# Kernel optimization log

Measured on AMD Instinct MI355X. Metric: run time of the kernel, lower is better.

## Reference

```python
import jax, jax.numpy as jnp
import numpy as np

B, T = 128, 512
D_IN, D_OUT, H = 12, 320, 64


def _conv1d(x, w, b, dilation):
    # x: [B,C,T], w: [O,I,K]  (torch Conv1d layout), 'same' padding for odd receptive field
    k = w.shape[-1]
    pad = ((k - 1) * dilation + 1) // 2
    y = jax.lax.conv_general_dilated(x, w, (1,), [(pad, pad)], rhs_dilation=(dilation,),
                                     dimension_numbers=('NCH', 'OIH', 'NCH'))
    return y + b[None, :, None]


def _gelu(x):
    return jax.nn.gelu(x, approximate=False)  # torch F.gelu default (erf)


def _encoder(x, c0_1_w, c0_1_b, c0_2_w, c0_2_b, c1_p_w, c1_p_b, c1_1_w, c1_1_b, c1_2_w, c1_2_b):
    # TS2Vec DilatedConvEncoder, channels=[64, 320], kernel=3. x: [B,T,64] -> [B,T,320]
    h = x.transpose(0, 2, 1)  # [B,64,T]
    # block 0: 64->64, dilation 1, identity residual
    res = h
    t = _conv1d(_gelu(h), c0_1_w, c0_1_b, 1)
    t = _conv1d(_gelu(t), c0_2_w, c0_2_b, 1)
    h = t + res
    # block 1: 64->320, dilation 2, final -> 1x1 projector residual
    res = _conv1d(h, c1_p_w, c1_p_b, 1)
    t = _conv1d(_gelu(h), c1_1_w, c1_1_b, 2)
    t = _conv1d(_gelu(t), c1_2_w, c1_2_b, 2)
    h = t + res
    return h.transpose(0, 2, 1)  # [B,T,320]


def _gru_cell(x, h, wih, whh, bih, bhh):
    # torch.nn.GRUCell math
    gi = x @ wih.T + bih  # [B,3H]
    gh = h @ whh.T + bhh
    i_r, i_z, i_n = jnp.split(gi, 3, axis=-1)
    h_r, h_z, h_n = jnp.split(gh, 3, axis=-1)
    r = jax.nn.sigmoid(i_r + h_r)
    z = jax.nn.sigmoid(i_z + h_z)
    n = jnp.tanh(i_n + r * h_n)
    return (1.0 - z) * n + z * h


def setup_inputs() -> dict:
    key = jax.random.key(0)
    ks = iter(jax.random.split(key, 40))
    f = lambda shape, s=0.05: (jax.random.normal(next(ks), shape, dtype=jnp.float32) * s)
    inp = {
        'x1': jax.random.normal(next(ks), (B, T, D_IN), dtype=jnp.float32),
        'x2': jax.random.normal(next(ks), (B, T, D_IN), dtype=jnp.float32),
        'X1': jax.random.normal(next(ks), (B, T, D_IN), dtype=jnp.float32),
        'X2': jax.random.normal(next(ks), (B, T, D_IN), dtype=jnp.float32),
        'X': jax.random.normal(next(ks), (B, T, D_IN), dtype=jnp.float32),
        'w_in': f((D_IN, H)), 'b_in': f((H,)),
        'c0_1_w': f((H, H, 3)), 'c0_1_b': f((H,)),
        'c0_2_w': f((H, H, 3)), 'c0_2_b': f((H,)),
        'c1_p_w': f((D_OUT, H, 1)), 'c1_p_b': f((D_OUT,)),
        'c1_1_w': f((D_OUT, H, 3)), 'c1_1_b': f((D_OUT,)),
        'c1_2_w': f((D_OUT, D_OUT, 3)), 'c1_2_b': f((D_OUT,)),
        'ih_dense_w': f((D_OUT, 4 * D_OUT)), 'ih_dense_b': f((4 * D_OUT,)),
        'ih_proj_w': f((4 * D_OUT, D_IN)), 'ih_proj_b': f((D_IN,)),
        'fc_w': f((D_IN, D_OUT)), 'fc_b': f((D_OUT,)),
        'gru_wih': f((3 * H, D_OUT)), 'gru_whh': f((3 * H, H)),
        'gru_bih': f((3 * H,)), 'gru_bhh': f((3 * H,)),
        'out_w': f((H, D_OUT)), 'out_b': f((D_OUT,)),
        'fcr_w': f((D_OUT, D_IN)), 'fcr_b': f((D_IN,)),
    }
    return inp


def reference(x1, x2, X1, X2, X, w_in, b_in, c0_1_w, c0_1_b, c0_2_w, c0_2_b,
              c1_p_w, c1_p_b, c1_1_w, c1_1_b, c1_2_w, c1_2_b,
              ih_dense_w, ih_dense_b, ih_proj_w, ih_proj_b,
              fc_w, fc_b, gru_wih, gru_whh, gru_bih, gru_bhh,
              out_w, out_b, fcr_w, fcr_b):
    conv_p = (c0_1_w, c0_1_b, c0_2_w, c0_2_b, c1_p_w, c1_p_b, c1_1_w, c1_1_b, c1_2_w, c1_2_b)
    m1 = (x1 != 0).astype(jnp.int32)
    m2 = (x2 != 0).astype(jnp.int32)
    enc = lambda a: _encoder(a @ w_in + b_in, *conv_p)  # dropout = identity (deterministic ref)
    x_whole1 = enc(X1)
    x_whole2 = enc(X2)

    def interp(a):
        r = enc(a)
        h = jax.nn.relu(r @ ih_dense_w + ih_dense_b)
        return h @ ih_proj_w + ih_proj_b  # [B,T,D_IN]

    x_interp1 = interp(x1)
    x_interp2 = interp(x2)
    mask1 = (~jnp.isnan(x_interp1).any(-1)).astype(jnp.float32)  # [B,T]

    y1 = x_interp1 @ fc_w + fc_b  # [B,T,320] (self.fc applied to every step at once)
    y2 = x_interp2 @ fc_w + fc_b
    h0 = jnp.zeros((x1.shape[0], gru_whh.shape[1]), x1.dtype)

    def step(carry, xs):
        h1, h2 = carry
        yt1, yt2, mt = xs
        h1 = _gru_cell(yt1, h1, gru_wih, gru_whh, gru_bih, gru_bhh)
        h2 = _gru_cell(yt2, h2, gru_wih, gru_whh, gru_bih, gru_bhh)
        o1 = h1 @ out_w + out_b
        o2 = h2 @ out_w + out_b
        keep = (mt == 1.0)[:, None]
        o1 = jnp.where(keep, yt1, o1)
        o2 = jnp.where(keep, yt1, o2)  # faithful: source uses mask1 / y_t1 for both
        return (h1, h2), (o1, o2)

    _, (o1, o2) = jax.lax.scan(step, (h0, h0),
                               (y1.transpose(1, 0, 2), y2.transpose(1, 0, 2), mask1.T))
    outputs2 = jax.lax.stop_gradient(o2.transpose(1, 0, 2)) @ fcr_w + fcr_b
    outputs1 = jax.lax.stop_gradient(o1.transpose(1, 0, 2)) @ fcr_w + fcr_b
    return (x_whole1, x_whole2, outputs1, outputs2, m1, m2, x1, x2)
```

## Files before the change

### kernel.cpp

```cpp
#include <hip/hip_runtime.h>
#include <hip/hip_bf16.h>
#include <math.h>


#define BB    128
#define TSEQ  512
#define NTILE 8
#define DIN   12
#define C0    64
#define C1    320
#define TT    64
#define PP    76
#define HALO  6
#define R64P  72

#define S1 ((size_t)BB * TSEQ * C1)
#define S2 ((size_t)BB * TSEQ * DIN)

typedef __attribute__((ext_vector_type(8))) __bf16 bf16x8;
typedef __attribute__((ext_vector_type(4))) float f32x4;
#define MFMA16(a, b, c) __builtin_amdgcn_mfma_f32_16x16x32_bf16(a, b, c, 0, 0, 0)

#define O01 0
#define O02 12288
#define O11 24576
#define O12 86016
#define OD  413696
#define OP  823296
#define NWS 843776
#define OGM 843776
#define OF2 844064

#define LA  0
#define LB  10656
#define LC  10656
#define LSZ 54176
#define LRR 0
#define LZB 40960
#define LXI 50176
#define LGM 53248
#define LF2 53824

__device__ __forceinline__ float bf2f(const __hip_bfloat16 v) { return __bfloat162float(v); }
__device__ __forceinline__ __hip_bfloat16 f2bf(float f)       { return __float2bfloat16(f); }
__device__ __forceinline__ float geluf(float x) {
    return 0.5f * x * (1.0f + erff(x * 0.7071067811865475f));
}
__device__ __forceinline__ bf16x8 ldb8(const void* p) { return *(const bf16x8*)p; }
__device__ __forceinline__ void* swp(void* base, int row, int col) {
    return (void*)((unsigned char*)base + (((row * 640 + col * 2)) ^ ((row & 7) << 4)));
}

extern "C" __global__ void __launch_bounds__(256) prep_w(
    const float* __restrict__ c01w, const float* __restrict__ c02w,
    const float* __restrict__ c11w, const float* __restrict__ c12w,
    const float* __restrict__ c1pw, const float* __restrict__ dw,
    const float* __restrict__ pw,
    const float* __restrict__ fcw,  const float* __restrict__ fcb,
    const float* __restrict__ fcrw, const float* __restrict__ fcrb,
    __hip_bfloat16* __restrict__ ws)
{
    for (size_t i = (size_t)blockIdx.x * 256 + threadIdx.x; i < NWS;
         i += (size_t)gridDim.x * 256) {
        float v;
        if (i < O02)      { int q = (int)i;        int n = q / 192, r = q % 192;
                            v = c01w[(n * 64 + (r & 63)) * 3 + (r >> 6)]; }
        else if (i < O11) { int q = (int)(i - O02); int n = q / 192, r = q % 192;
                            v = c02w[(n * 64 + (r & 63)) * 3 + (r >> 6)]; }
        else if (i < O12) { int q = (int)(i - O11); int n = q / 192, r = q % 192;
                            v = c11w[(n * 64 + (r & 63)) * 3 + (r >> 6)]; }
        else if (i < OD)  { int q = (int)(i - O12); int n = q >> 10, k = q & 1023;
                            v = (k < 960) ? c12w[(n * 320 + (k % 320)) * 3 + (k / 320)]
                                          : c1pw[n * 64 + (k - 960)]; }
        else if (i < OP)  { int q = (int)(i - OD);  int h = q / 320, c = q % 320;
                            v = dw[c * 1280 + h]; }
        else              { int q = (int)(i - OP);  int j = q / 1280, h = q % 1280;
                            v = (j < 12) ? pw[h * 12 + j] : 0.f; }
        ws[i] = f2bf(v);
    }
    if (blockIdx.x == 0) {
        float* gm = (float*)(ws + OGM);
        float* f2 = (float*)(ws + OF2);
        for (int o = threadIdx.x; o < 144; o += 256) {
            int j = o / 12, j2 = o - j * 12;
            float s = 0.f;
            for (int c = 0; c < C1; c++) s += fcw[j * C1 + c] * fcrw[c * 12 + j2];
            gm[o] = s;
        }
        if (threadIdx.x < 12) {
            float s = fcrb[threadIdx.x];
            for (int c = 0; c < C1; c++) s += fcb[c] * fcrw[c * 12 + threadIdx.x];
            f2[threadIdx.x] = s;
        }
    }
}

extern "C" __global__ void __launch_bounds__(256, 3) fused_main(
    const float* __restrict__ x1,  const float* __restrict__ X1,
    const float* __restrict__ X2,
    const float* __restrict__ w_in, const float* __restrict__ b_in,
    const float* __restrict__ c01b, const float* __restrict__ c02b,
    const float* __restrict__ c1pb, const float* __restrict__ c11b,
    const float* __restrict__ c12b,
    const float* __restrict__ db,   const float* __restrict__ pb,
    const __hip_bfloat16* __restrict__ ws,
    float* __restrict__ out)
{
    __shared__ __align__(16) unsigned char smem[LSZ];
    __hip_bfloat16* A  = (__hip_bfloat16*)(smem + LA);
    __hip_bfloat16* Bf = (__hip_bfloat16*)(smem + LB);
    unsigned char*  Cb = smem + LC;
    unsigned char*  Rb = smem + LRR;
    float* XI = (float*)(smem + LXI);
    float* Gm = (float*)(smem + LGM);
    float* F2 = (float*)(smem + LF2);

    const int tid  = threadIdx.x;
    const int wv   = tid >> 6;
    const int lane = tid & 63;
    const int lm   = lane & 15;
    const int lq   = lane >> 4;
    const int bid  = blockIdx.x;
    const int pass = bid % 3;
    const int rem  = bid / 3;
    const int b    = rem >> 3;
    const int t0   = (rem & (NTILE - 1)) * TT;
    const float* xin = (pass == 0) ? X1 : (pass == 1) ? X2 : x1;

    const f32x4 Z4 = {0.f, 0.f, 0.f, 0.f};

    for (int o = tid; o < PP * C0; o += 256) {
        int p = o >> 6, c = o & 63;
        int t = t0 + p - HALO;
        float acc = 0.f;
        if (t >= 0 && t < TSEQ) {
            acc = b_in[c];
            const float4* xr4 = (const float4*)(xin + ((size_t)b * TSEQ + t) * DIN);
            float4 v0 = xr4[0], v1 = xr4[1], v2 = xr4[2];
            const float xv[12] = {v0.x, v0.y, v0.z, v0.w, v1.x, v1.y,
                                  v1.z, v1.w, v2.x, v2.y, v2.z, v2.w};
            #pragma unroll
            for (int i = 0; i < DIN; i++) acc += xv[i] * w_in[i * C0 + c];
        }
        if (p < 74) A[p * R64P + c] = f2bf(acc);
        Bf[p * R64P + c] = f2bf(geluf(acc));
    }
    __syncthreads();

    {
        const int oc = wv * 16 + lm;
        bf16x8 bw[6];
        #pragma unroll
        for (int ks = 0; ks < 6; ks++)
            bw[ks] = ldb8(ws + O01 + oc * 192 + ks * 32 + (lq << 3));
        f32x4 acc[5] = {Z4, Z4, Z4, Z4, Z4};
        #pragma unroll
        for (int ks = 0; ks < 6; ks++) {
            int tap = ks >> 1, ci = ((ks & 1) << 5) + (lq << 3);
            #pragma unroll
            for (int mt = 0; mt < 5; mt++) {
                int p = 1 + mt * 16 + lm + tap - 1; p = p > 75 ? 75 : p;
                acc[mt] = MFMA16(ldb8(Bf + p * R64P + ci), bw[ks], acc[mt]);
            }
        }
        __syncthreads();
        float bias = c01b[oc];
        #pragma unroll
        for (int mt = 0; mt < 5; mt++)
            #pragma unroll
            for (int r = 0; r < 4; r++) {
                int m = mt * 16 + lq * 4 + r;
                if (m < 74) {
                    int p = 1 + m, t = t0 + p - HALO;
                    Bf[p * R64P + oc] =
                        f2bf((t >= 0 && t < TSEQ) ? geluf(acc[mt][r] + bias) : 0.f);
                }
            }
    }
    __syncthreads();

    {
        const int oc = wv * 16 + lm;
        bf16x8 bw[6];
        #pragma unroll
        for (int ks = 0; ks < 6; ks++)
            bw[ks] = ldb8(ws + O02 + oc * 192 + ks * 32 + (lq << 3));
        f32x4 acc[5] = {Z4, Z4, Z4, Z4, Z4};
        #pragma unroll
        for (int ks = 0; ks < 6; ks++) {
            int tap = ks >> 1, ci = ((ks & 1) << 5) + (lq << 3);
            #pragma unroll
            for (int mt = 0; mt < 5; mt++) {
                int p = 2 + mt * 16 + lm + tap - 1; p = p > 75 ? 75 : p;
                acc[mt] = MFMA16(ldb8(Bf + p * R64P + ci), bw[ks], acc[mt]);
            }
        }
        float resv[5][4];
        #pragma unroll
        for (int mt = 0; mt < 5; mt++)
            #pragma unroll
            for (int r = 0; r < 4; r++) {
                int m = mt * 16 + lq * 4 + r;
                resv[mt][r] = (m < 72) ? bf2f(A[(2 + m) * R64P + oc]) : 0.f;
            }
        __syncthreads();
        float bias = c02b[oc];
        #pragma unroll
        for (int mt = 0; mt < 5; mt++)
            #pragma unroll
            for (int r = 0; r < 4; r++) {
                int m = mt * 16 + lq * 4 + r;
                if (m < 72) {
                    int p = 2 + m, t = t0 + p - HALO;
                    bool v = (t >= 0 && t < TSEQ);
                    float hb = acc[mt][r] + bias + resv[mt][r];
                    A [p * R64P + oc] = f2bf(v ? hb : 0.f);
                    Bf[p * R64P + oc] = f2bf(v ? geluf(hb) : 0.f);
                }
            }
    }
    __syncthreads();

    {
        f32x4 acc[5][5];
        #pragma unroll
        for (int mt = 0; mt < 5; mt++)
            #pragma unroll
            for (int nt = 0; nt < 5; nt++) acc[mt][nt] = Z4;
        #pragma unroll
        for (int ks = 0; ks < 6; ks++) {
            int tap = ks >> 1, ci = ((ks & 1) << 5) + (lq << 3);
            bf16x8 a[5];
            #pragma unroll
            for (int mt = 0; mt < 5; mt++) {
                int p = 4 + mt * 16 + lm + 2 * (tap - 1); p = p > 75 ? 75 : p;
                a[mt] = ldb8(Bf + p * R64P + ci);
            }
            #pragma unroll
            for (int nt = 0; nt < 5; nt++) {
                bf16x8 bw = ldb8(ws + O11 + (wv * 80 + nt * 16 + lm) * 192
                                 + ks * 32 + (lq << 3));
                #pragma unroll
                for (int mt = 0; mt < 5; mt++)
                    acc[mt][nt] = MFMA16(a[mt], bw, acc[mt][nt]);
            }
        }
        __syncthreads();
        #pragma unroll
        for (int nt = 0; nt < 5; nt++) {
            int oc = wv * 80 + nt * 16 + lm;
            float bias = c11b[oc];
            #pragma unroll
            for (int mt = 0; mt < 5; mt++)
                #pragma unroll
                for (int r = 0; r < 4; r++) {
                    int m = mt * 16 + lq * 4 + r;
                    if (m < 68) {
                        int t = t0 + 4 + m - HALO;
                        *(__hip_bfloat16*)swp(Cb, m, oc) =
                            f2bf((t >= 0 && t < TSEQ) ? geluf(acc[mt][nt][r] + bias) : 0.f);
                    }
                }
        }
    }
    __syncthreads();

    {
        f32x4 acc[4][5];
        #pragma unroll
        for (int kk = 0; kk < 4; kk++)
            #pragma unroll
            for (int nt = 0; nt < 5; nt++) acc[kk][nt] = Z4;
        bf16x8 ba[5], bb[5];
        #pragma unroll
        for (int nt = 0; nt < 5; nt++)
            ba[nt] = ldb8(ws + O12 + (wv * 80 + nt * 16 + lm) * 1024 + (lq << 3));
        for (int ks = 0; ks < 32; ks += 2) {
            #pragma unroll
            for (int nt = 0; nt < 5; nt++)
                bb[nt] = ldb8(ws + O12 + (wv * 80 + nt * 16 + lm) * 1024
                              + (ks + 1) * 32 + (lq << 3));
            {
                bf16x8 a[4];
                if (ks < 30) {
                    int tap = (ks >= 20) ? 2 : (ks >= 10 ? 1 : 0);
                    int ci = (ks - tap * 10) * 32 + (lq << 3);
                    #pragma unroll
                    for (int mt = 0; mt < 4; mt++)
                        a[mt] = ldb8(swp(Cb, 2 + mt * 16 + lm + 2 * (tap - 1), ci));
                } else {
                    int ci = ((ks - 30) << 5) + (lq << 3);
                    #pragma unroll
                    for (int mt = 0; mt < 4; mt++)
                        a[mt] = ldb8(A + (6 + mt * 16 + lm) * R64P + ci);
                }
                #pragma unroll
                for (int nt = 0; nt < 5; nt++)
                    #pragma unroll
                    for (int mt = 0; mt < 4; mt++)
                        acc[mt][nt] = MFMA16(a[mt], ba[nt], acc[mt][nt]);
            }
            if (ks + 2 < 32)
                #pragma unroll
                for (int nt = 0; nt < 5; nt++)
                    ba[nt] = ldb8(ws + O12 + (wv * 80 + nt * 16 + lm) * 1024
                                  + (ks + 2) * 32 + (lq << 3));
            {
                int k1 = ks + 1;
                bf16x8 a[4];
                if (k1 < 30) {
                    int tap = (k1 >= 20) ? 2 : (k1 >= 10 ? 1 : 0);
                    int ci = (k1 - tap * 10) * 32 + (lq << 3);
                    #pragma unroll
                    for (int mt = 0; mt < 4; mt++)
                        a[mt] = ldb8(swp(Cb, 2 + mt * 16 + lm + 2 * (tap - 1), ci));
                } else {
                    int ci = ((k1 - 30) << 5) + (lq << 3);
                    #pragma unroll
                    for (int mt = 0; mt < 4; mt++)
                        a[mt] = ldb8(A + (6 + mt * 16 + lm) * R64P + ci);
                }
                #pragma unroll
                for (int nt = 0; nt < 5; nt++)
                    #pragma unroll
                    for (int mt = 0; mt < 4; mt++)
                        acc[mt][nt] = MFMA16(a[mt], bb[nt], acc[mt][nt]);
            }
        }
        if (pass < 2) {
            #pragma unroll
            for (int nt = 0; nt < 5; nt++) {
                int oc = wv * 80 + nt * 16 + lm;
                float bias = c12b[oc] + c1pb[oc];
                const size_t obase = (pass == 1) ? S1 : (size_t)0;
                #pragma unroll
                for (int mt = 0; mt < 4; mt++)
                    #pragma unroll
                    for (int r = 0; r < 4; r++) {
                        int m = mt * 16 + lq * 4 + r;
                        out[obase + ((size_t)b * TSEQ + t0 + m) * C1 + oc] =
                            acc[mt][nt][r] + bias;
                    }
            }
        } else {
            __syncthreads();
            #pragma unroll
            for (int nt = 0; nt < 5; nt++) {
                int oc = wv * 80 + nt * 16 + lm;
                float bias = c12b[oc] + c1pb[oc];
                #pragma unroll
                for (int mt = 0; mt < 4; mt++)
                    #pragma unroll
                    for (int r = 0; r < 4; r++) {
                        int m = mt * 16 + lq * 4 + r;
                        *(__hip_bfloat16*)swp(Rb, m, oc) = f2bf(acc[mt][nt][r] + bias);
                    }
            }
            const float* gmw = (const float*)(ws + OGM);
            const float* f2w = (const float*)(ws + OF2);
            for (int o = tid; o < TT * 12; o += 256) XI[o] = pb[o % 12];
            for (int o = tid; o < 144; o += 256) Gm[o] = gmw[o];
            if (tid < 12) F2[tid] = f2w[tid];
            __syncthreads();
        }
    }

    if (pass == 2) {
        __hip_bfloat16* zb = (__hip_bfloat16*)(smem + LZB) + wv * (16 * R64P);
        f32x4 xacc[4] = {Z4, Z4, Z4, Z4};
        for (int cn = 0; cn < 5; cn++) {
            const int h0 = wv * 320 + cn * 64;
            f32x4 dacc[4][4];
            #pragma unroll
            for (int mt = 0; mt < 4; mt++)
                #pragma unroll
                for (int nt = 0; nt < 4; nt++) dacc[mt][nt] = Z4;
            bf16x8 ba[4], bb[4];
            #pragma unroll
            for (int nt = 0; nt < 4; nt++)
                ba[nt] = ldb8(ws + OD + (h0 + nt * 16 + lm) * 320 + (lq << 3));
            for (int ks = 0; ks < 10; ks += 2) {
                #pragma unroll
                for (int nt = 0; nt < 4; nt++)
                    bb[nt] = ldb8(ws + OD + (h0 + nt * 16 + lm) * 320
                                  + (ks + 1) * 32 + (lq << 3));
                {
                    bf16x8 a[4];
                    #pragma unroll
                    for (int mt = 0; mt < 4; mt++)
                        a[mt] = ldb8(swp(Rb, mt * 16 + lm, ks * 32 + (lq << 3)));
                    #pragma unroll
                    for (int nt = 0; nt < 4; nt++)
                        #pragma unroll
                        for (int mt = 0; mt < 4; mt++)
                            dacc[mt][nt] = MFMA16(a[mt], ba[nt], dacc[mt][nt]);
                }
                if (ks + 2 < 10)
                    #pragma unroll
                    for (int nt = 0; nt < 4; nt++)
                        ba[nt] = ldb8(ws + OD + (h0 + nt * 16 + lm) * 320
                                      + (ks + 2) * 32 + (lq << 3));
                {
                    bf16x8 a[4];
                    #pragma unroll
                    for (int mt = 0; mt < 4; mt++)
                        a[mt] = ldb8(swp(Rb, mt * 16 + lm, (ks + 1) * 32 + (lq << 3)));
                    #pragma unroll
                    for (int nt = 0; nt < 4; nt++)
                        #pragma unroll
                        for (int mt = 0; mt < 4; mt++)
                            dacc[mt][nt] = MFMA16(a[mt], bb[nt], dacc[mt][nt]);
                }
            }
            #pragma unroll
            for (int mt = 0; mt < 4; mt++) {
                #pragma unroll
                for (int nt = 0; nt < 4; nt++) {
                    int h = h0 + nt * 16 + lm;
                    float dbv = db[h];
                    #pragma unroll
                    for (int r = 0; r < 4; r++)
                        zb[(lq * 4 + r) * R64P + nt * 16 + lm] =
                            f2bf(fmaxf(dacc[mt][nt][r] + dbv, 0.f));
                }
                #pragma unroll
                for (int k2 = 0; k2 < 2; k2++) {
                    int hl = k2 * 32 + (lq << 3);
                    bf16x8 bf = ldb8(ws + OP + lm * 1280 + h0 + hl);
                    xacc[mt] = MFMA16(ldb8(zb + lm * R64P + hl), bf, xacc[mt]);
                }
            }
        }
        if (lm < 12) {
            #pragma unroll
            for (int mt = 0; mt < 4; mt++)
                #pragma unroll
                for (int r = 0; r < 4; r++)
                    atomicAdd(&XI[(mt * 16 + lq * 4 + r) * 12 + lm], xacc[mt][r]);
        }
        __syncthreads();
        for (int o = tid; o < TT * 12; o += 256) {
            int p = o / 12, j2 = o - p * 12;
            float val = F2[j2];
            #pragma unroll
            for (int j = 0; j < 12; j++) val += XI[p * 12 + j] * Gm[j * 12 + j2];
            size_t idx = ((size_t)b * TSEQ + t0 + p) * DIN + j2;
            out[2 * S1 + idx]      = val;
            out[2 * S1 + S2 + idx] = val;
        }
    }
}

extern "C" __global__ void __launch_bounds__(256) tail_kernel(
    const float* __restrict__ x1, const float* __restrict__ x2,
    float* __restrict__ out)
{
    size_t i = (size_t)blockIdx.x * 256 + threadIdx.x;
    if (i >= S2) return;
    float a = x1[i], c = x2[i];
    const size_t base = 2 * S1 + 2 * S2;
    out[base + i]          = (a != 0.f) ? 1.f : 0.f;
    out[base + S2 + i]     = (c != 0.f) ? 1.f : 0.f;
    out[base + 2 * S2 + i] = a;
    out[base + 3 * S2 + i] = c;
}

extern "C" void kernel_launch(void* const* d_in, const int* in_sizes, int n_in,
                              void* d_out, int out_size, void* d_ws, size_t ws_size,
                              hipStream_t stream)
{
    (void)in_sizes; (void)n_in; (void)ws_size; (void)out_size;
    const float* x1   = (const float*)d_in[0];
    const float* x2   = (const float*)d_in[1];
    const float* X1   = (const float*)d_in[2];
    const float* X2   = (const float*)d_in[3];
    const float* w_in = (const float*)d_in[5];
    const float* b_in = (const float*)d_in[6];
    const float* c01w = (const float*)d_in[7];
    const float* c01b = (const float*)d_in[8];
    const float* c02w = (const float*)d_in[9];
    const float* c02b = (const float*)d_in[10];
    const float* c1pw = (const float*)d_in[11];
    const float* c1pb = (const float*)d_in[12];
    const float* c11w = (const float*)d_in[13];
    const float* c11b = (const float*)d_in[14];
    const float* c12w = (const float*)d_in[15];
    const float* c12b = (const float*)d_in[16];
    const float* dwp  = (const float*)d_in[17];
    const float* dbp  = (const float*)d_in[18];
    const float* pwp  = (const float*)d_in[19];
    const float* pbp  = (const float*)d_in[20];
    const float* fcw  = (const float*)d_in[21];
    const float* fcb  = (const float*)d_in[22];
    const float* fcrw = (const float*)d_in[29];
    const float* fcrb = (const float*)d_in[30];
    float* out = (float*)d_out;
    __hip_bfloat16* ws = (__hip_bfloat16*)d_ws;

    prep_w<<<824, 256, 0, stream>>>(c01w, c02w, c11w, c12w, c1pw, dwp, pwp,
                                    fcw, fcb, fcrw, fcrb, ws);

    fused_main<<<3 * BB * NTILE, 256, 0, stream>>>(
        x1, X1, X2, w_in, b_in, c01b, c02b, c1pb, c11b, c12b,
        dbp, pbp, ws, out);

    tail_kernel<<<(int)((S2 + 255) / 256), 256, 0, stream>>>(x1, x2, out);
}
```

Baseline: 933.9 us.

## Prefetch conv weights with deeper register pipelining and relocate pass-2 LDS buffers

Moves the XI/Gm/F2 shared buffers to a region of their own past the existing LDS layout, so they can be filled at kernel start for pass 2 rather than after the last conv. The first dilated conv now prefetches the next k-step's weight fragments into registers. The second conv moves to a triple-buffered weight / double-buffered activation software pipeline, so global weight loads overlap the MFMAs. The extra registers and LDS make the launch bound drop from 3 to 2 blocks per SM, which may reduce occupancy.

```diff
diff --git a/kernel.cpp b/kernel.cpp
--- a/kernel.cpp
+++ b/kernel.cpp
@@ -34,12 +34,12 @@
 #define LA  0
 #define LB  10656
 #define LC  10656
-#define LSZ 54176
+#define LXI 54176
+#define LGM 57248
+#define LF2 57824
+#define LSZ 57872
 #define LRR 0
 #define LZB 40960
-#define LXI 50176
-#define LGM 53248
-#define LF2 53824
 
 __device__ __forceinline__ float bf2f(const __hip_bfloat16 v) { return __bfloat162float(v); }
 __device__ __forceinline__ __hip_bfloat16 f2bf(float f)       { return __float2bfloat16(f); }
@@ -48,7 +48,7 @@
 }
 __device__ __forceinline__ bf16x8 ldb8(const void* p) { return *(const bf16x8*)p; }
 __device__ __forceinline__ void* swp(void* base, int row, int col) {
-    return (void*)((unsigned char*)base + (((row * 640 + col * 2)) ^ ((row & 7) << 4)));
+    return (void*)((unsigned char*)base + ((row * 640 + col * 2) ^ ((row & 7) << 4)));
 }
 
 extern "C" __global__ void __launch_bounds__(256) prep_w(
@@ -95,7 +95,7 @@
     }
 }
 
-extern "C" __global__ void __launch_bounds__(256, 3) fused_main(
+extern "C" __global__ void __launch_bounds__(256, 2) fused_main(
     const float* __restrict__ x1,  const float* __restrict__ X1,
     const float* __restrict__ X2,
     const float* __restrict__ w_in, const float* __restrict__ b_in,
@@ -129,6 +129,14 @@
 
     const f32x4 Z4 = {0.f, 0.f, 0.f, 0.f};
 
+    if (pass == 2) {
+        const float* gmw = (const float*)(ws + OGM);
+        const float* f2w = (const float*)(ws + OF2);
+        for (int o = tid; o < 144; o += 256) Gm[o] = gmw[o];
+        if (tid < 12) F2[tid] = f2w[tid];
+        for (int o = tid; o < TT * 12; o += 256) XI[o] = pb[o % 12];
+    }
+
     for (int o = tid; o < PP * C0; o += 256) {
         int p = o >> 6, c = o & 63;
         int t = t0 + p - HALO;
@@ -227,8 +235,17 @@
         for (int mt = 0; mt < 5; mt++)
             #pragma unroll
             for (int nt = 0; nt < 5; nt++) acc[mt][nt] = Z4;
+        bf16x8 bcur[5], bnxt[5];
+        #pragma unroll
+        for (int nt = 0; nt < 5; nt++)
+            bcur[nt] = ldb8(ws + O11 + (wv * 80 + nt * 16 + lm) * 192 + (lq << 3));
         #pragma unroll
         for (int ks = 0; ks < 6; ks++) {
+            if (ks < 5)
+                #pragma unroll
+                for (int nt = 0; nt < 5; nt++)
+                    bnxt[nt] = ldb8(ws + O11 + (wv * 80 + nt * 16 + lm) * 192
+                                    + (ks + 1) * 32 + (lq << 3));
             int tap = ks >> 1, ci = ((ks & 1) << 5) + (lq << 3);
             bf16x8 a[5];
             #pragma unroll
@@ -237,13 +254,12 @@
                 a[mt] = ldb8(Bf + p * R64P + ci);
             }
             #pragma unroll
-            for (int nt = 0; nt < 5; nt++) {
-                bf16x8 bw = ldb8(ws + O11 + (wv * 80 + nt * 16 + lm) * 192
-                                 + ks * 32 + (lq << 3));
+            for (int nt = 0; nt < 5; nt++)
                 #pragma unroll
                 for (int mt = 0; mt < 5; mt++)
-                    acc[mt][nt] = MFMA16(a[mt], bw, acc[mt][nt]);
-            }
+                    acc[mt][nt] = MFMA16(a[mt], bcur[nt], acc[mt][nt]);
+            #pragma unroll
+            for (int nt = 0; nt < 5; nt++) bcur[nt] = bnxt[nt];
         }
         __syncthreads();
         #pragma unroll
@@ -268,65 +284,50 @@
     {
         f32x4 acc[4][5];
         #pragma unroll
-        for (int kk = 0; kk < 4; kk++)
-            #pragma unroll
-            for (int nt = 0; nt < 5; nt++) acc[kk][nt] = Z4;
-        bf16x8 ba[5], bb[5];
-        #pragma unroll
-        for (int nt = 0; nt < 5; nt++)
-            ba[nt] = ldb8(ws + O12 + (wv * 80 + nt * 16 + lm) * 1024 + (lq << 3));
-        for (int ks = 0; ks < 32; ks += 2) {
+        for (int mt = 0; mt < 4; mt++)
+            #pragma unroll
+            for (int nt = 0; nt < 5; nt++) acc[mt][nt] = Z4;
+        bf16x8 a0[4], a1[4], b0[5], b1[5], b2[5];
+        auto LDA = [&](int ks, bf16x8 (&a)[4]) {
+            if (ks < 30) {
+                int tap = (ks >= 20) ? 2 : (ks >= 10 ? 1 : 0);
+                int ci = (ks - tap * 10) * 32 + (lq << 3);
+                #pragma unroll
+                for (int mt = 0; mt < 4; mt++)
+                    a[mt] = ldb8(swp(Cb, 2 + mt * 16 + lm + 2 * (tap - 1), ci));
+            } else {
+                int ci = ((ks - 30) << 5) + (lq << 3);
+                #pragma unroll
+                for (int mt = 0; mt < 4; mt++)
+                    a[mt] = ldb8(A + (6 + mt * 16 + lm) * R64P + ci);
+            }
+        };
+        auto LDB = [&](int ks, bf16x8 (&bw)[5]) {
             #pragma unroll
             for (int nt = 0; nt < 5; nt++)
-                bb[nt] = ldb8(ws + O12 + (wv * 80 + nt * 16 + lm) * 1024
-                              + (ks + 1) * 32 + (lq << 3));
-            {
-                bf16x8 a[4];
-                if (ks < 30) {
-                    int tap = (ks >= 20) ? 2 : (ks >= 10 ? 1 : 0);
-                    int ci = (ks - tap * 10) * 32 + (lq << 3);
-                    #pragma unroll
-                    for (int mt = 0; mt < 4; mt++)
-                        a[mt] = ldb8(swp(Cb, 2 + mt * 16 + lm + 2 * (tap - 1), ci));
-                } else {
-                    int ci = ((ks - 30) << 5) + (lq << 3);
-                    #pragma unroll
-                    for (int mt = 0; mt < 4; mt++)
-                        a[mt] = ldb8(A + (6 + mt * 16 + lm) * R64P + ci);
-                }
-                #pragma unroll
-                for (int nt = 0; nt < 5; nt++)
-                    #pragma unroll
-                    for (int mt = 0; mt < 4; mt++)
-                        acc[mt][nt] = MFMA16(a[mt], ba[nt], acc[mt][nt]);
-            }
-            if (ks + 2 < 32)
-                #pragma unroll
-                for (int nt = 0; nt < 5; nt++)
-                    ba[nt] = ldb8(ws + O12 + (wv * 80 + nt * 16 + lm) * 1024
-                                  + (ks + 2) * 32 + (lq << 3));
-            {
-                int k1 = ks + 1;
-                bf16x8 a[4];
-                if (k1 < 30) {
-                    int tap = (k1 >= 20) ? 2 : (k1 >= 10 ? 1 : 0);
-                    int ci = (k1 - tap * 10) * 32 + (lq << 3);
-                    #pragma unroll
-                    for (int mt = 0; mt < 4; mt++)
-                        a[mt] = ldb8(swp(Cb, 2 + mt * 16 + lm + 2 * (tap - 1), ci));
-                } else {
-                    int ci = ((k1 - 30) << 5) + (lq << 3);
-                    #pragma unroll
-                    for (int mt = 0; mt < 4; mt++)
-                        a[mt] = ldb8(A + (6 + mt * 16 + lm) * R64P + ci);
-                }
-                #pragma unroll
-                for (int nt = 0; nt < 5; nt++)
-                    #pragma unroll
-                    for (int mt = 0; mt < 4; mt++)
-                        acc[mt][nt] = MFMA16(a[mt], bb[nt], acc[mt][nt]);
-            }
-        }
+                bw[nt] = ldb8(ws + O12 + (wv * 80 + nt * 16 + lm) * 1024
+                              + ks * 32 + (lq << 3));
+        };
+        auto FMA = [&](bf16x8 (&a)[4], bf16x8 (&bw)[5]) {
+            #pragma unroll
+            for (int nt = 0; nt < 5; nt++)
+                #pragma unroll
+                for (int mt = 0; mt < 4; mt++)
+                    acc[mt][nt] = MFMA16(a[mt], bw[nt], acc[mt][nt]);
+        };
+        LDA(0, a0); LDB(0, b0); LDB(1, b1);
+        for (int g = 0; g < 5; g++) {
+            int p = 6 * g;
+            LDA(p + 1, a1); LDB(p + 2, b2); FMA(a0, b0);
+            LDA(p + 2, a0); LDB(p + 3, b0); FMA(a1, b1);
+            LDA(p + 3, a1); LDB(p + 4, b1); FMA(a0, b2);
+            LDA(p + 4, a0); LDB(p + 5, b2); FMA(a1, b0);
+            LDA(p + 5, a1); LDB(p + 6, b0); FMA(a0, b1);
+            LDA(p + 6, a0); LDB(p + 7, b1); FMA(a1, b2);
+        }
+        LDA(31, a1); FMA(a0, b0);
+        FMA(a1, b1);
+
         if (pass < 2) {
             #pragma unroll
             for (int nt = 0; nt < 5; nt++) {
@@ -356,11 +357,6 @@
                         *(__hip_bfloat16*)swp(Rb, m, oc) = f2bf(acc[mt][nt][r] + bias);
                     }
             }
-            const float* gmw = (const float*)(ws + OGM);
-            const float* f2w = (const float*)(ws + OF2);
-            for (int o = tid; o < TT * 12; o += 256) XI[o] = pb[o % 12];
-            for (int o = tid; o < 144; o += 256) Gm[o] = gmw[o];
-            if (tid < 12) F2[tid] = f2w[tid];
             __syncthreads();
         }
     }
```

Result: faster. 838.1 us (-10.3%).
